# Performance work log

Measured on AMD Instinct MI355X. Metric: run time of the kernel, lower is better.

The kernel has to match this reference:

```python
import jax, jax.numpy as jnp
import numpy as np

DEPTH, DIM, HEADS, EXP = 6, 768, 12, 4
B, N = 8, 1024
EPS = 1e-5


def setup_inputs() -> dict:
    key = jax.random.key(0)
    ks = jax.random.split(key, 6)
    s = 0.02
    inp = {
        "x": jax.random.normal(ks[0], (B, N, DIM), dtype=jnp.float32),
        "ln1_g": jnp.ones((DEPTH, DIM), jnp.float32),
        "ln1_b": jnp.zeros((DEPTH, DIM), jnp.float32),
        "wqkv": jax.random.normal(ks[1], (DEPTH, DIM, 3 * DIM), jnp.float32) * s,
        "bqkv": jnp.zeros((DEPTH, 3 * DIM), jnp.float32),
        "ln2_g": jnp.ones((DEPTH, DIM), jnp.float32),
        "ln2_b": jnp.zeros((DEPTH, DIM), jnp.float32),
        "w1": jax.random.normal(ks[2], (DEPTH, DIM, EXP * DIM), jnp.float32) * s,
        "b1": jnp.zeros((DEPTH, EXP * DIM), jnp.float32),
        "w2": jax.random.normal(ks[3], (DEPTH, EXP * DIM, DIM), jnp.float32) * s,
        "b2": jnp.zeros((DEPTH, DIM), jnp.float32),
    }
    return inp


def _layernorm(x, g, b):
    mu = jnp.mean(x, axis=-1, keepdims=True)
    var = jnp.mean(jnp.square(x - mu), axis=-1, keepdims=True)
    return (x - mu) * jax.lax.rsqrt(var + EPS) * g + b


def _block(x, p):
    ln1_g, ln1_b, wqkv, bqkv, ln2_g, ln2_b, w1, b1, w2, b2 = p
    # --- attention (pre-norm, residual) ---
    x1 = _layernorm(x, ln1_g, ln1_b)
    qkv = x1 @ wqkv + bqkv  # [b, n, 3*dim]
    q, k, v = jnp.split(qkv, 3, axis=-1)
    dh = DIM // HEADS
    def heads(t):  # b n (h d) -> b h n d
        return t.reshape(B, N, HEADS, dh).transpose(0, 2, 1, 3)
    q, k, v = heads(q), heads(k), heads(v)
    scale = DIM ** (-0.5)  # NB: module scales by full dim, not head dim
    dots = jnp.einsum("bhnd,bhmd->bhnm", q, k) * scale
    attn = jax.nn.softmax(dots, axis=-1)
    out = jnp.einsum("bhnm,bhmd->bhnd", attn, v)
    out = out.transpose(0, 2, 1, 3).reshape(B, N, DIM)
    x = x + out
    # --- feedforward (pre-norm, residual) ---
    x2 = _layernorm(x, ln2_g, ln2_b)
    h = jax.nn.gelu(x2 @ w1 + b1, approximate=False)
    x = x + (h @ w2 + b2)
    return x


def reference(x, ln1_g, ln1_b, wqkv, bqkv, ln2_g, ln2_b, w1, b1, w2, b2):
    params = (ln1_g, ln1_b, wqkv, bqkv, ln2_g, ln2_b, w1, b1, w2, b2)

    def body(carry, p):
        return _block(carry, p), None

    x, _ = jax.lax.scan(body, x, params)
    return x
```

## Files before the change

### kernel.cpp

```cpp
#include <hip/hip_runtime.h>
#include <hip/hip_bf16.h>
#include <math.h>

#define DEPTH 6
#define DIM   768
#define HEADS 12
#define DH    64
#define NCTX  1024
#define BATCH 8
#define ROWS  (BATCH*NCTX)
#define DIM3  (3*DIM)
#define DIMF  (4*DIM)
#define LNEPS 1e-5f

typedef __attribute__((ext_vector_type(8)))  short short8;
typedef __attribute__((ext_vector_type(4)))  float floatx4;
typedef __attribute__((ext_vector_type(16))) float floatx16;
using bf16 = __hip_bfloat16;
typedef unsigned int u32;

static __device__ __forceinline__ bf16 f2bf(float v){ return __float2bfloat16(v); }
static __device__ __forceinline__ float bf2f(unsigned short u){
    union { unsigned int i; float f; } c; c.i = ((unsigned int)u) << 16; return c.f;
}
static __device__ __forceinline__ unsigned short bfu(float v){ return __bfloat16_as_ushort(f2bf(v)); }
static __device__ __forceinline__ u32 pk2(float a, float b){
    return (u32)bfu(a) | ((u32)bfu(b) << 16);
}

static __device__ __forceinline__ void gl_lds16(const void* g, void* l) {
    __builtin_amdgcn_global_load_lds((const __attribute__((address_space(1))) void*)g,
                                     (__attribute__((address_space(3))) void*)l, 16, 0, 0);
}

__global__ void k_transpose_convert(const float* __restrict__ W, bf16* __restrict__ WT,
                                    int K, int N) {
    __shared__ float tile[32][33];
    int l = blockIdx.z;
    const float* Wl = W + (size_t)l * K * N;
    bf16* WTl = WT + (size_t)l * K * N;
    int n0 = blockIdx.x * 32, k0 = blockIdx.y * 32;
    int tx = threadIdx.x, ty = threadIdx.y;
#pragma unroll
    for (int i = 0; i < 4; i++)
        tile[ty + i*8][tx] = Wl[(size_t)(k0 + ty + i*8) * N + n0 + tx];
    __syncthreads();
#pragma unroll
    for (int i = 0; i < 4; i++)
        WTl[(size_t)(n0 + ty + i*8) * K + k0 + tx] = f2bf(tile[tx][ty + i*8]);
}

__global__ __launch_bounds__(256) void k_layernorm(const float* __restrict__ x,
                                                   const float* __restrict__ g,
                                                   const float* __restrict__ b,
                                                   bf16* __restrict__ y) {
    int row  = blockIdx.x * 4 + (threadIdx.x >> 6);
    int lane = threadIdx.x & 63;
    const float4* xr = (const float4*)(x + (size_t)row * DIM);
    float4 v[3];
    float s = 0.f, s2 = 0.f;
#pragma unroll
    for (int i = 0; i < 3; i++) {
        v[i] = xr[lane + i*64];
        s  += v[i].x + v[i].y + v[i].z + v[i].w;
        s2 += v[i].x*v[i].x + v[i].y*v[i].y + v[i].z*v[i].z + v[i].w*v[i].w;
    }
#pragma unroll
    for (int m = 1; m < 64; m <<= 1) { s += __shfl_xor(s, m); s2 += __shfl_xor(s2, m); }
    float mu  = s * (1.f / DIM);
    float var = s2 * (1.f / DIM) - mu * mu;
    float rs  = rsqrtf(var + LNEPS);
    bf16* yr = y + (size_t)row * DIM;
    const float4* g4 = (const float4*)g;
    const float4* b4 = (const float4*)b;
#pragma unroll
    for (int i = 0; i < 3; i++) {
        float4 gg = g4[lane + i*64], bb = b4[lane + i*64];
        float r0 = (v[i].x - mu) * rs * gg.x + bb.x;
        float r1 = (v[i].y - mu) * rs * gg.y + bb.y;
        float r2 = (v[i].z - mu) * rs * gg.z + bb.z;
        float r3 = (v[i].w - mu) * rs * gg.w + bb.w;
        uint2 u; u.x = pk2(r0, r1); u.y = pk2(r2, r3);
        *(uint2*)&yr[4 * (lane + i*64)] = u;
    }
}

template<int MODE, int BM, int BN>
__global__ __launch_bounds__(256, 2) void k_gemm(const bf16* __restrict__ A,
                                                 const bf16* __restrict__ WT,
                                                 const float* __restrict__ bias,
                                                 bf16* __restrict__ outb,
                                                 float* __restrict__ outf,
                                                 int N, int K) {
    constexpr int IF  = BM / 32;
    constexpr int JF  = BN / 32;
    constexpr int LPT = BM / 64 + BN / 64;
    __shared__ __align__(16) bf16 As[3][BM*32];
    __shared__ __align__(16) bf16 Bs[3][BN*32];
    int nt = N / BN;
    int nwg = gridDim.x;
    int fblk = blockIdx.x;
    int swz = (fblk & 7) * (nwg >> 3) + (fblk >> 3);
    int m0 = (swz / nt) * BM, n0 = (swz % nt) * BN;
    int t = threadIdx.x;
    int lane = t & 63, w = t >> 6;
    int wr = (w >> 1) * (BM / 2), wc = (w & 1) * (BN / 2);
    int lr = lane & 15, lg = lane >> 4;
    int fcol = (lg ^ ((lane >> 1) & 3)) * 8;

    floatx4 acc[IF][JF] = {};
    int NT = K >> 5;

    auto STAGE = [&](int ks, int buf) {
        int ko = ks << 5;
#pragma unroll
        for (int ac = 0; ac < BM/64; ac++) {
            int c = ac*256 + t;
            int row = c >> 2, col = ((c & 3) ^ ((c >> 3) & 3)) * 8;
            gl_lds16(A + (size_t)(m0 + row) * K + ko + col, &As[buf][c * 8]);
        }
#pragma unroll
        for (int bc = 0; bc < BN/64; bc++) {
            int c = bc*256 + t;
            int row = c >> 2, col = ((c & 3) ^ ((c >> 3) & 3)) * 8;
            gl_lds16(WT + (size_t)(n0 + row) * K + ko + col, &Bs[buf][c * 8]);
        }
    };
    auto WAITC = [&]() {
        if constexpr (LPT == 6)      asm volatile("s_waitcnt vmcnt(6)" ::: "memory");
        else if constexpr (LPT == 4) asm volatile("s_waitcnt vmcnt(4)" ::: "memory");
        else                         asm volatile("s_waitcnt vmcnt(3)" ::: "memory");
    };

    STAGE(0, 0);
    STAGE(1, 1);
    WAITC();
    __builtin_amdgcn_s_barrier();

    for (int kb = 0; kb < NT; kb += 3) {
#pragma unroll
        for (int s = 0; s < 3; s++) {
            int ks = kb + s;
            bool pf = (ks + 2) < NT;
            if (pf) STAGE(ks + 2, (s + 2) % 3);
            short8 af[IF], bfr[JF];
#pragma unroll
            for (int i = 0; i < IF; i++) af[i]  = *(const short8*)&As[s][(wr + i*16 + lr)*32 + fcol];
#pragma unroll
            for (int j = 0; j < JF; j++) bfr[j] = *(const short8*)&Bs[s][(wc + j*16 + lr)*32 + fcol];
            __builtin_amdgcn_s_setprio(1);
#pragma unroll
            for (int i = 0; i < IF; i++)
#pragma unroll
                for (int j = 0; j < JF; j++)
                    acc[i][j] = __builtin_amdgcn_mfma_f32_16x16x32_bf16(af[i], bfr[j], acc[i][j], 0, 0, 0);
            __builtin_amdgcn_s_setprio(0);
            if (pf) WAITC();
            else    asm volatile("s_waitcnt vmcnt(0)" ::: "memory");
            __builtin_amdgcn_s_barrier();
        }
    }
#pragma unroll
    for (int i = 0; i < IF; i++)
#pragma unroll
        for (int j = 0; j < JF; j++)
#pragma unroll
            for (int r = 0; r < 4; r++) {
                int row = m0 + wr + i*16 + lg*4 + r;
                int col = n0 + wc + j*16 + lr;
                float vv = acc[i][j][r] + bias[col];
                if (MODE == 0) {
                    outb[(size_t)row * N + col] = f2bf(vv);
                } else if (MODE == 1) {
                    float u = 1.5957691216f * (vv + 0.044715f * vv * vv * vv);
                    float gs = 1.f / (1.f + __expf(-u));
                    outb[(size_t)row * N + col] = f2bf(vv * gs);
                } else {
                    outf[(size_t)row * N + col] += vv;
                }
            }
}

static __device__ __forceinline__ int vt_off(int d, int k) {
    int dw = d * 36 + (k >> 1);
    dw ^= (d & 0x38) >> 1;
    return dw * 2 + (k & 1);
}

__global__ __launch_bounds__(256, 3) void k_attn(const bf16* __restrict__ qkv,
                                                 float* __restrict__ x) {
    int f = blockIdx.x;
    int b  = f & 7;
    int rr = f >> 3;
    int h  = rr % 12;
    int qt = rr / 12;
    int t = threadIdx.x, lane = t & 63, w = t >> 6;
    int q = lane & 31, hi = lane >> 5;
    const size_t bn0 = (size_t)b * NCTX;
    const bf16* Qg = qkv + bn0 * DIM3 + h * DH;
    const bf16* Kg = Qg + DIM;
    const bf16* Vg = Qg + 2 * DIM;
    int q0 = qt * 128 + w * 32;

    const float qs = 0.036084391824351615f * 1.4426950408889634f;
    short8 qf[4];
#pragma unroll
    for (int s = 0; s < 4; s++) {
        short8 raw = *(const short8*)&Qg[(size_t)(q0 + q) * DIM3 + s*16 + hi*8];
        short8 o;
#pragma unroll
        for (int e = 0; e < 8; e++)
            o[e] = (short)bfu(bf2f((unsigned short)raw[e]) * qs);
        qf[s] = o;
    }

    __shared__ __align__(16) bf16 KsS[64*64];
    __shared__ __align__(16) bf16 VTs[64*72];
    __shared__ float wbc[4][32];

    u32* ksw = (u32*)KsS;

    int sr[2], sc[2];
#pragma unroll
    for (int it = 0; it < 2; it++) { int c = it*256 + t; sr[it] = c >> 3; sc[it] = (c & 7) * 8; }

    floatx16 pacc[2] = {};
    float mrow = -3e38f, lrow = 0.f;

    uint4 kreg[2], vreg[2];
#pragma unroll
    for (int it = 0; it < 2; it++) {
        kreg[it] = *(const uint4*)&Kg[(size_t)sr[it] * DIM3 + sc[it]];
        vreg[it] = *(const uint4*)&Vg[(size_t)sr[it] * DIM3 + sc[it]];
    }

    for (int kt = 0; kt < 16; kt++) {
        __syncthreads();
#pragma unroll
        for (int it = 0; it < 2; it++) {
            int row = sr[it], u = sc[it] >> 3;
            *(uint4*)(ksw + row*32 + ((u ^ (row & 7)) << 2)) = kreg[it];
            const bf16* vp = (const bf16*)&vreg[it];
#pragma unroll
            for (int e = 0; e < 8; e++) VTs[vt_off(sc[it] + e, row)] = vp[e];
        }
        __syncthreads();
        if (kt + 1 < 16) {
            int kv0 = (kt + 1) * 64;
#pragma unroll
            for (int it = 0; it < 2; it++) {
                kreg[it] = *(const uint4*)&Kg[(size_t)(kv0 + sr[it]) * DIM3 + sc[it]];
                vreg[it] = *(const uint4*)&Vg[(size_t)(kv0 + sr[it]) * DIM3 + sc[it]];
            }
        }

        floatx16 sacc[2] = {};
        __builtin_amdgcn_s_setprio(1);
#pragma unroll
        for (int kb = 0; kb < 2; kb++) {
#pragma unroll
            for (int s = 0; s < 4; s++) {
                int row = kb*32 + q;
                short8 kf = *(const short8*)(ksw + row*32 + (((2*s + hi) ^ (row & 7)) << 2));
                sacc[kb] = __builtin_amdgcn_mfma_f32_32x32x16_bf16(kf, qf[s], sacc[kb], 0, 0, 0);
            }
        }
        __builtin_amdgcn_s_setprio(0);

        float mx = sacc[0][0];
#pragma unroll
        for (int r = 1; r < 16; r++) mx = fmaxf(mx, sacc[0][r]);
#pragma unroll
        for (int r = 0; r < 16; r++) mx = fmaxf(mx, sacc[1][r]);
        mx = fmaxf(mx, __shfl_xor(mx, 32));
        bool chg = mx > mrow + 8.f;
        if (__any(chg)) {
            float mnew = chg ? mx : mrow;
            float corr = exp2f(mrow - mnew);
            mrow = mnew;
            lrow *= corr;
            wbc[w][q] = corr;
#pragma unroll
            for (int r = 0; r < 16; r++) {
                float c = wbc[w][(r & 3) + 8*(r >> 2) + 4*hi];
                pacc[0][r] *= c; pacc[1][r] *= c;
            }
        }

        float sum = 0.f;
#pragma unroll
        for (int kb = 0; kb < 2; kb++) {
            float pf[16];
#pragma unroll
            for (int r = 0; r < 16; r++) { pf[r] = exp2f(sacc[kb][r] - mrow); sum += pf[r]; }
#pragma unroll
            for (int g = 0; g < 2; g++) {
                u32 a0 = pk2(pf[8*g+0], pf[8*g+1]);
                u32 a1 = pk2(pf[8*g+2], pf[8*g+3]);
                u32 b0 = pk2(pf[8*g+4], pf[8*g+5]);
                u32 b1 = pk2(pf[8*g+6], pf[8*g+7]);
                asm volatile("v_permlane32_swap_b32 %0, %1" : "+v"(a0), "+v"(b0));
                asm volatile("v_permlane32_swap_b32 %0, %1" : "+v"(a1), "+v"(b1));
                union { u32 u[4]; short8 s8; } pa;
                pa.u[0] = a0; pa.u[1] = a1; pa.u[2] = b0; pa.u[3] = b1;
                int ks = 2*kb + g;
                __builtin_amdgcn_s_setprio(1);
#pragma unroll
                for (int db = 0; db < 2; db++) {
                    short8 vb = *(const short8*)&VTs[vt_off(db*32 + q, 16*ks + 8*hi)];
                    pacc[db] = __builtin_amdgcn_mfma_f32_32x32x16_bf16(pa.s8, vb, pacc[db], 0, 0, 0);
                }
                __builtin_amdgcn_s_setprio(0);
            }
        }
        sum += __shfl_xor(sum, 32);
        lrow += sum;
    }

    wbc[w][q] = 1.f / lrow;
    float* xr = x + bn0 * DIM + (size_t)h * DH;
#pragma unroll
    for (int r = 0; r < 16; r++) {
        int qrow = (r & 3) + 8*(r >> 2) + 4*hi;
        float li = wbc[w][qrow];
#pragma unroll
        for (int db = 0; db < 2; db++) {
            int col = db*32 + q;
            xr[(size_t)(q0 + qrow) * DIM + col] += pacc[db][r] * li;
        }
    }
}

extern "C" void kernel_launch(void* const* d_in, const int* in_sizes, int n_in,
                              void* d_out, int out_size, void* d_ws, size_t ws_size,
                              hipStream_t stream) {
    const float* x_in  = (const float*)d_in[0];
    const float* ln1_g = (const float*)d_in[1];
    const float* ln1_b = (const float*)d_in[2];
    const float* wqkv  = (const float*)d_in[3];
    const float* bqkv  = (const float*)d_in[4];
    const float* ln2_g = (const float*)d_in[5];
    const float* ln2_b = (const float*)d_in[6];
    const float* w1    = (const float*)d_in[7];
    const float* b1    = (const float*)d_in[8];
    const float* w2    = (const float*)d_in[9];
    const float* b2    = (const float*)d_in[10];
    float* x = (float*)d_out;

    char* ws = (char*)d_ws;
    size_t off = 0;
    auto alloc = [&](size_t bytes) { void* p = ws + off; off += (bytes + 255) & ~255ull; return p; };
    bf16* wqkvT = (bf16*)alloc((size_t)DEPTH * DIM * DIM3 * 2);
    bf16* w1T   = (bf16*)alloc((size_t)DEPTH * DIM * DIMF * 2);
    bf16* w2T   = (bf16*)alloc((size_t)DEPTH * DIMF * DIM * 2);
    bf16* xn    = (bf16*)alloc((size_t)ROWS * DIM * 2);
    bf16* qkvh  = (bf16*)alloc((size_t)ROWS * DIMF * 2);
    if (off > ws_size) return;

    hipMemcpyAsync(x, x_in, (size_t)ROWS * DIM * 4, hipMemcpyDeviceToDevice, stream);

    k_transpose_convert<<<dim3(DIM3/32, DIM/32,  DEPTH), dim3(32, 8), 0, stream>>>(wqkv, wqkvT, DIM,  DIM3);
    k_transpose_convert<<<dim3(DIMF/32, DIM/32,  DEPTH), dim3(32, 8), 0, stream>>>(w1,   w1T,   DIM,  DIMF);
    k_transpose_convert<<<dim3(DIM/32,  DIMF/32, DEPTH), dim3(32, 8), 0, stream>>>(w2,   w2T,   DIMF, DIM);

    for (int l = 0; l < DEPTH; l++) {
        k_layernorm<<<ROWS/4, 256, 0, stream>>>(x, ln1_g + l*DIM, ln1_b + l*DIM, xn);
        k_gemm<0,256,128><<<dim3((DIM3/128)*(ROWS/256)), 256, 0, stream>>>(
            xn, wqkvT + (size_t)l*DIM*DIM3, bqkv + (size_t)l*DIM3, qkvh, nullptr, DIM3, DIM);
        k_attn<<<dim3(768), 256, 0, stream>>>(qkvh, x);
        k_layernorm<<<ROWS/4, 256, 0, stream>>>(x, ln2_g + l*DIM, ln2_b + l*DIM, xn);
        k_gemm<1,256,128><<<dim3((DIMF/128)*(ROWS/256)), 256, 0, stream>>>(
            xn, w1T + (size_t)l*DIM*DIMF, b1 + (size_t)l*DIMF, qkvh, nullptr, DIMF, DIM);
        k_gemm<2,128,64><<<dim3((DIM/64)*(ROWS/128)), 256, 0, stream>>>(
            qkvh, w2T + (size_t)l*DIMF*DIM, b2 + (size_t)l*DIM, nullptr, x, DIM, DIMF);
    }
}
```

Measured before the change: 1.627 ms.

## Write V transposed from QKV GEMM and double-buffer K/V via direct-to-LDS loads

The QKV GEMM epilogue now writes the V slice in a per-head transposed [b,h,d,n] layout into a new workspace buffer. This lets the attention kernel load both K and V straight into swizzled LDS with async global-to-LDS copies. The attention kernel switches to a two-stage LDS double buffer that prefetches the next tile while computing the current one, removing the per-element V transpose scatter and one barrier per step. The trade-offs are more LDS per block, which may reduce occupancy at launch_bounds 3, and a strided transposed store in the GEMM epilogue. It also relies on a gl_lds16 helper assumed to be defined in the unseen part of the file.

```diff
diff --git a/kernel.cpp b/kernel.cpp
--- a/kernel.cpp
+++ b/kernel.cpp
@@ -91,6 +91,7 @@
                                                  const float* __restrict__ bias,
                                                  bf16* __restrict__ outb,
                                                  float* __restrict__ outf,
+                                                 bf16* __restrict__ vT,
                                                  int N, int K) {
     constexpr int IF  = BM / 32;
     constexpr int JF  = BN / 32;
@@ -163,31 +164,38 @@
 #pragma unroll
     for (int i = 0; i < IF; i++)
 #pragma unroll
-        for (int j = 0; j < JF; j++)
-#pragma unroll
-            for (int r = 0; r < 4; r++) {
-                int row = m0 + wr + i*16 + lg*4 + r;
-                int col = n0 + wc + j*16 + lr;
-                float vv = acc[i][j][r] + bias[col];
-                if (MODE == 0) {
-                    outb[(size_t)row * N + col] = f2bf(vv);
-                } else if (MODE == 1) {
-                    float u = 1.5957691216f * (vv + 0.044715f * vv * vv * vv);
-                    float gs = 1.f / (1.f + __expf(-u));
-                    outb[(size_t)row * N + col] = f2bf(vv * gs);
-                } else {
-                    outf[(size_t)row * N + col] += vv;
+        for (int j = 0; j < JF; j++) {
+            int row0 = m0 + wr + i*16 + lg*4;
+            int col  = n0 + wc + j*16 + lr;
+            float bz = bias[col];
+            float vv[4];
+#pragma unroll
+            for (int r = 0; r < 4; r++) vv[r] = acc[i][j][r] + bz;
+            if (MODE == 0 && n0 >= 2*DIM) {
+                int h = (col - 2*DIM) >> 6, d = (col - 2*DIM) & 63;
+                int bb = row0 >> 10, n = row0 & 1023;
+                uint2 u; u.x = pk2(vv[0], vv[1]); u.y = pk2(vv[2], vv[3]);
+                *(uint2*)(vT + (((size_t)bb*12 + h)*64 + d)*1024 + n) = u;
+            } else {
+#pragma unroll
+                for (int r = 0; r < 4; r++) {
+                    if (MODE == 0) {
+                        outb[(size_t)(row0+r) * N + col] = f2bf(vv[r]);
+                    } else if (MODE == 1) {
+                        float vx = vv[r];
+                        float u = 1.5957691216f * (vx + 0.044715f * vx * vx * vx);
+                        float gs = 1.f / (1.f + __expf(-u));
+                        outb[(size_t)(row0+r) * N + col] = f2bf(vx * gs);
+                    } else {
+                        outf[(size_t)(row0+r) * N + col] += vv[r];
+                    }
                 }
             }
-}
-
-static __device__ __forceinline__ int vt_off(int d, int k) {
-    int dw = d * 36 + (k >> 1);
-    dw ^= (d & 0x38) >> 1;
-    return dw * 2 + (k & 1);
+        }
 }
 
 __global__ __launch_bounds__(256, 3) void k_attn(const bf16* __restrict__ qkv,
+                                                 const bf16* __restrict__ vT,
                                                  float* __restrict__ x) {
     int f = blockIdx.x;
     int b  = f & 7;
@@ -199,8 +207,26 @@
     const size_t bn0 = (size_t)b * NCTX;
     const bf16* Qg = qkv + bn0 * DIM3 + h * DH;
     const bf16* Kg = Qg + DIM;
-    const bf16* Vg = Qg + 2 * DIM;
+    const bf16* Vt = vT + (((size_t)b*12 + h) * 64) * 1024;
     int q0 = qt * 128 + w * 32;
+
+    __shared__ __align__(16) bf16 Kb[2][64*64];
+    __shared__ __align__(16) bf16 Vb[2][64*64];
+    __shared__ float wbc[4][32];
+
+    auto STAGE_KV = [&](int kt2, int buf) {
+        int kv0 = kt2 * 64;
+#pragma unroll
+        for (int it = 0; it < 2; it++) {
+            int i = it*256 + t;
+            int r8 = i >> 3;
+            int ulog = (i & 7) ^ (r8 & 7);
+            gl_lds16(Kg + (size_t)(kv0 + r8) * DIM3 + ulog*8, &Kb[buf][i*8]);
+            gl_lds16(Vt + (size_t)r8 * 1024 + kv0 + ulog*8,   &Vb[buf][i*8]);
+        }
+    };
+
+    STAGE_KV(0, 0);
 
     const float qs = 0.036084391824351615f * 1.4426950408889634f;
     short8 qf[4];
@@ -214,45 +240,18 @@
         qf[s] = o;
     }
 
-    __shared__ __align__(16) bf16 KsS[64*64];
-    __shared__ __align__(16) bf16 VTs[64*72];
-    __shared__ float wbc[4][32];
-
-    u32* ksw = (u32*)KsS;
-
-    int sr[2], sc[2];
-#pragma unroll
-    for (int it = 0; it < 2; it++) { int c = it*256 + t; sr[it] = c >> 3; sc[it] = (c & 7) * 8; }
-
     floatx16 pacc[2] = {};
     float mrow = -3e38f, lrow = 0.f;
 
-    uint4 kreg[2], vreg[2];
-#pragma unroll
-    for (int it = 0; it < 2; it++) {
-        kreg[it] = *(const uint4*)&Kg[(size_t)sr[it] * DIM3 + sc[it]];
-        vreg[it] = *(const uint4*)&Vg[(size_t)sr[it] * DIM3 + sc[it]];
-    }
+    asm volatile("s_waitcnt vmcnt(0)" ::: "memory");
+    __builtin_amdgcn_s_barrier();
 
     for (int kt = 0; kt < 16; kt++) {
-        __syncthreads();
-#pragma unroll
-        for (int it = 0; it < 2; it++) {
-            int row = sr[it], u = sc[it] >> 3;
-            *(uint4*)(ksw + row*32 + ((u ^ (row & 7)) << 2)) = kreg[it];
-            const bf16* vp = (const bf16*)&vreg[it];
-#pragma unroll
-            for (int e = 0; e < 8; e++) VTs[vt_off(sc[it] + e, row)] = vp[e];
-        }
-        __syncthreads();
-        if (kt + 1 < 16) {
-            int kv0 = (kt + 1) * 64;
-#pragma unroll
-            for (int it = 0; it < 2; it++) {
-                kreg[it] = *(const uint4*)&Kg[(size_t)(kv0 + sr[it]) * DIM3 + sc[it]];
-                vreg[it] = *(const uint4*)&Vg[(size_t)(kv0 + sr[it]) * DIM3 + sc[it]];
-            }
-        }
+        int cur = kt & 1;
+        if (kt + 1 < 16) STAGE_KV(kt + 1, cur ^ 1);
+
+        u32* ksw = (u32*)&Kb[cur][0];
+        u32* vsw = (u32*)&Vb[cur][0];
 
         floatx16 sacc[2] = {};
         __builtin_amdgcn_s_setprio(1);
@@ -307,7 +306,8 @@
                 __builtin_amdgcn_s_setprio(1);
 #pragma unroll
                 for (int db = 0; db < 2; db++) {
-                    short8 vb = *(const short8*)&VTs[vt_off(db*32 + q, 16*ks + 8*hi)];
+                    int dd = db*32 + q;
+                    short8 vb = *(const short8*)(vsw + dd*32 + (((2*ks + hi) ^ (dd & 7)) << 2));
                     pacc[db] = __builtin_amdgcn_mfma_f32_32x32x16_bf16(pa.s8, vb, pacc[db], 0, 0, 0);
                 }
                 __builtin_amdgcn_s_setprio(0);
@@ -315,6 +315,9 @@
         }
         sum += __shfl_xor(sum, 32);
         lrow += sum;
+
+        asm volatile("s_waitcnt vmcnt(0)" ::: "memory");
+        __builtin_amdgcn_s_barrier();
     }
 
     wbc[w][q] = 1.f / lrow;
@@ -355,6 +358,7 @@
     bf16* w2T   = (bf16*)alloc((size_t)DEPTH * DIMF * DIM * 2);
     bf16* xn    = (bf16*)alloc((size_t)ROWS * DIM * 2);
     bf16* qkvh  = (bf16*)alloc((size_t)ROWS * DIMF * 2);
+    bf16* vTb   = (bf16*)alloc((size_t)BATCH * HEADS * DH * NCTX * 2);
     if (off > ws_size) return;
 
     hipMemcpyAsync(x, x_in, (size_t)ROWS * DIM * 4, hipMemcpyDeviceToDevice, stream);
@@ -366,12 +370,12 @@
     for (int l = 0; l < DEPTH; l++) {
         k_layernorm<<<ROWS/4, 256, 0, stream>>>(x, ln1_g + l*DIM, ln1_b + l*DIM, xn);
         k_gemm<0,256,128><<<dim3((DIM3/128)*(ROWS/256)), 256, 0, stream>>>(
-            xn, wqkvT + (size_t)l*DIM*DIM3, bqkv + (size_t)l*DIM3, qkvh, nullptr, DIM3, DIM);
-        k_attn<<<dim3(768), 256, 0, stream>>>(qkvh, x);
+            xn, wqkvT + (size_t)l*DIM*DIM3, bqkv + (size_t)l*DIM3, qkvh, nullptr, vTb, DIM3, DIM);
+        k_attn<<<dim3(768), 256, 0, stream>>>(qkvh, vTb, x);
         k_layernorm<<<ROWS/4, 256, 0, stream>>>(x, ln2_g + l*DIM, ln2_b + l*DIM, xn);
         k_gemm<1,256,128><<<dim3((DIMF/128)*(ROWS/256)), 256, 0, stream>>>(
-            xn, w1T + (size_t)l*DIM*DIMF, b1 + (size_t)l*DIMF, qkvh, nullptr, DIMF, DIM);
+            xn, w1T + (size_t)l*DIM*DIMF, b1 + (size_t)l*DIMF, qkvh, nullptr, nullptr, DIMF, DIM);
         k_gemm<2,128,64><<<dim3((DIM/64)*(ROWS/128)), 256, 0, stream>>>(
-            qkvh, w2T + (size_t)l*DIMF*DIM, b2 + (size_t)l*DIM, nullptr, x, DIM, DIMF);
-    }
-}
+            qkvh, w2T + (size_t)l*DIMF*DIM, b2 + (size_t)l*DIM, nullptr, x, nullptr, DIM, DIMF);
+    }
+}
```

Result: no change. 1.603 ms (-1.5%).
